# Kernel tuning notes

Hardware: AMD Instinct MI355X
Metric: run time of the kernel (lower is better)

The kernel has to match this reference:

```python
import jax, jax.numpy as jnp
import numpy as np

B, N, D, H = 1, 4096, 1024, 16
HD = D // H  # head_dim = 64


def setup_inputs() -> dict:
    key = jax.random.key(0)
    ks = jax.random.split(key, 5)
    s = 0.02
    return {
        "x": jax.random.normal(ks[0], (B, N, D), dtype=jnp.float32),
        "Wq": jax.random.normal(ks[1], (D, D), dtype=jnp.float32) * s,
        "Wk": jax.random.normal(ks[2], (D, D), dtype=jnp.float32) * s,
        "Wv": jax.random.normal(ks[3], (D, D), dtype=jnp.float32) * s,
        "Wo": jax.random.normal(ks[4], (D, D), dtype=jnp.float32) * s,
        "bo": jnp.zeros((D,), dtype=jnp.float32),
    }


def reference(x, Wq, Wk, Wv, Wo, bo):
    b, n, d = x.shape
    # QKV projections -> [b, h, n, hd]
    def proj(W):
        return jnp.einsum("bnd,de->bne", x, W).reshape(b, n, H, HD).transpose(0, 2, 1, 3)
    q, k, v = proj(Wq), proj(Wk), proj(Wv)
    # Scores [b, h, n, n] with causal mask (matches masked_fill with triu(diag=1))
    scores = jnp.einsum("bhqd,bhkd->bhqk", q, k)
    causal = jnp.tril(jnp.ones((n, n), dtype=bool))
    scores = jnp.where(causal, scores, -jnp.inf)
    attn = jax.nn.softmax(scores / jnp.sqrt(jnp.float32(HD)), axis=-1)
    # dropout p=0.0 -> identity
    ctx = jnp.einsum("bhqk,bhkd->bhqd", attn, v)
    ctx = ctx.transpose(0, 2, 1, 3).reshape(b, n, d)
    return jnp.einsum("bnd,de->bne", ctx, Wo) + bo
```

## Files before the change

kernel.cpp:

```cpp
#include <hip/hip_runtime.h>


#define N_TOK 4096
#define DMODEL 1024
#define NH 16
#define HDIM 64

typedef __bf16 bf16x8 __attribute__((ext_vector_type(8)));
typedef __bf16 bf16x2v __attribute__((ext_vector_type(2)));
typedef short short4v __attribute__((ext_vector_type(4)));
typedef unsigned int uint2v __attribute__((ext_vector_type(2)));
typedef float f32x4 __attribute__((ext_vector_type(4)));

__device__ __forceinline__ unsigned short f2bf(float f) {
  unsigned u = __builtin_bit_cast(unsigned, f);
  u += 0x7FFFu + ((u >> 16) & 1u);
  return (unsigned short)(u >> 16);
}

__device__ __forceinline__ float bf2f(unsigned short u) {
  unsigned x = (unsigned)u << 16;
  return __builtin_bit_cast(float, x);
}

__device__ __forceinline__ unsigned pack2bf(float f0, float f1) {
  unsigned a = __builtin_bit_cast(unsigned, f0);
  unsigned b = __builtin_bit_cast(unsigned, f1);
  a += 0x7FFFu + ((a >> 16) & 1u);
  b += 0x7FFFu + ((b >> 16) & 1u);
  return (a >> 16) | (b & 0xFFFF0000u);
}

__device__ __forceinline__ unsigned packpk(float f0, float f1) {
#if defined(__HIP_DEVICE_COMPILE__) && __has_builtin(__builtin_amdgcn_cvt_pk_bf16_f32)
  bf16x2v r = __builtin_amdgcn_cvt_pk_bf16_f32(f0, f1);
  return __builtin_bit_cast(unsigned, r);
#else
  return pack2bf(f0, f1);
#endif
}

__device__ __forceinline__ float fast_exp2(float x) {
#if defined(__HIP_DEVICE_COMPILE__)
#if __has_builtin(__builtin_amdgcn_exp2f)
  return __builtin_amdgcn_exp2f(x);
#else
  float r;
  asm("v_exp_f32 %0, %1" : "=v"(r) : "v"(x));
  return r;
#endif
#else
  return exp2f(x);
#endif
}

__device__ __forceinline__ f32x4 mfma16x16x16(short4v a, short4v b, f32x4 c) {
#if defined(__HIP_DEVICE_COMPILE__)
#if __has_builtin(__builtin_amdgcn_mfma_f32_16x16x16bf16_1k)
  return __builtin_amdgcn_mfma_f32_16x16x16bf16_1k(a, b, c, 0, 0, 0);
#else
  asm volatile("v_mfma_f32_16x16x16_bf16 %0, %1, %2, %0\n\ts_nop 7\n\ts_nop 1"
               : "+v"(c) : "v"(a), "v"(b));
  return c;
#endif
#else
  return c;
#endif
}

__device__ __forceinline__ void gll16(const unsigned short* g, unsigned short* l) {
#if defined(__HIP_DEVICE_COMPILE__)
  __builtin_amdgcn_global_load_lds((const __attribute__((address_space(1))) void*)g,
                                   (__attribute__((address_space(3))) void*)l, 16, 0, 0);
#endif
}

__global__ __launch_bounds__(256) void prep_kernel(
    const float* __restrict__ x, unsigned short* __restrict__ xb,
    const float* __restrict__ Wq, const float* __restrict__ Wk,
    const float* __restrict__ Wv, const float* __restrict__ Wo,
    unsigned short* __restrict__ Wqt, unsigned short* __restrict__ Wkt,
    unsigned short* __restrict__ Wvt, unsigned short* __restrict__ Wot) {
  const int bx = blockIdx.x;
  if (bx < 4096) {
    const int i = (bx * 256 + threadIdx.x) * 4;
    float4 v = *(const float4*)(x + i);
    ushort4 o;
    o.x = f2bf(v.x); o.y = f2bf(v.y); o.z = f2bf(v.z); o.w = f2bf(v.w);
    *(ushort4*)(xb + i) = o;
    return;
  }
  __shared__ float t[32][33];
  const int r = bx - 4096;
  const int z = r >> 10, rem = r & 1023;
  const int by = rem >> 5, bxx = rem & 31;
  const float* src;
  unsigned short* dst;
  switch (z) {
    case 0: src = Wq; dst = Wqt; break;
    case 1: src = Wk; dst = Wkt; break;
    case 2: src = Wv; dst = Wvt; break;
    default: src = Wo; dst = Wot; break;
  }
  const int tx = threadIdx.x & 31, ty = threadIdx.x >> 5;
  const int xx = bxx * 32 + tx;
  const int y0 = by * 32;
#pragma unroll
  for (int i = 0; i < 32; i += 8) t[ty + i][tx] = src[(y0 + ty + i) * DMODEL + xx];
  __syncthreads();
  const int ox = by * 32 + tx;
  const int oy0 = bxx * 32;
#pragma unroll
  for (int i = 0; i < 32; i += 8) dst[(oy0 + ty + i) * DMODEL + ox] = f2bf(t[tx][ty + i]);
}

__global__ __launch_bounds__(256) void gemm_qkv_kernel(
    const unsigned short* __restrict__ xb,
    const unsigned short* __restrict__ Wqt, const unsigned short* __restrict__ Wkt,
    const unsigned short* __restrict__ Wvt,
    unsigned short* __restrict__ Qg, unsigned short* __restrict__ Kg,
    unsigned short* __restrict__ Vtg) {
  __shared__ unsigned short As[128 * 32];
  __shared__ unsigned short Bs[128 * 32];
  __shared__ unsigned short Tt[64 * 132];
  const int z = blockIdx.z;
  const unsigned short* Bmat = (z == 0) ? Wqt : ((z == 1) ? Wkt : Wvt);
  const int tid = threadIdx.x, lane = tid & 63, wv = tid >> 6;
  const int quad = lane >> 4, l15 = lane & 15;
  const int wm = wv >> 1, wn = wv & 1;
  const int tm0 = blockIdx.y * 128, tn0 = blockIdx.x * 128;
  const int lrow = lane >> 2, lcol = (lane & 3) * 8;
  const f32x4 zero4 = {0.f, 0.f, 0.f, 0.f};
  f32x4 acc[4][4];
#pragma unroll
  for (int i = 0; i < 4; ++i)
#pragma unroll
    for (int j = 0; j < 4; ++j) acc[i][j] = zero4;

  for (int kb = 0; kb < DMODEL; kb += 32) {
#pragma unroll
    for (int r = 0; r < 2; ++r) {
      const int row0 = r * 64 + wv * 16;
      gll16(&xb[(tm0 + row0 + lrow) * DMODEL + kb + lcol], &As[row0 * 32]);
      gll16(&Bmat[(tn0 + row0 + lrow) * DMODEL + kb + lcol], &Bs[row0 * 32]);
    }
    __syncthreads();
    bf16x8 af[4], bfr[4];
#pragma unroll
    for (int i = 0; i < 4; ++i) {
      af[i]  = *(const bf16x8*)&As[(wm * 64 + i * 16 + l15) * 32 + quad * 8];
      bfr[i] = *(const bf16x8*)&Bs[(wn * 64 + i * 16 + l15) * 32 + quad * 8];
    }
#pragma unroll
    for (int mt = 0; mt < 4; ++mt)
#pragma unroll
      for (int nt = 0; nt < 4; ++nt)
        acc[mt][nt] = __builtin_amdgcn_mfma_f32_16x16x32_bf16(af[mt], bfr[nt], acc[mt][nt], 0, 0, 0);
    __syncthreads();
  }

  const float qs = 0.125f * 1.44269504088896f;
  if (z < 2) {
#pragma unroll
    for (int mt = 0; mt < 4; ++mt)
#pragma unroll
      for (int nt = 0; nt < 4; ++nt)
#pragma unroll
        for (int r = 0; r < 4; ++r) {
          const int row = tm0 + wm * 64 + mt * 16 + quad * 4 + r;
          const int col = tn0 + wn * 64 + nt * 16 + l15;
          const float v = acc[mt][nt][r];
          const int hh = col >> 6, hd = col & 63;
          if (z == 0) Qg[(hh * N_TOK + row) * HDIM + hd] = f2bf(v * qs);
          else        Kg[(hh * N_TOK + row) * HDIM + hd] = f2bf(v);
        }
  } else {
#pragma unroll 1
    for (int p = 0; p < 2; ++p) {
      if (wn == p) {
#pragma unroll
        for (int mt = 0; mt < 4; ++mt)
#pragma unroll
          for (int nt = 0; nt < 4; ++nt) {
            const int c = nt * 16 + l15;
#pragma unroll
            for (int r = 0; r < 4; ++r)
              Tt[c * 132 + wm * 64 + mt * 16 + quad * 4 + r] = f2bf(acc[mt][nt][r]);
          }
      }
      __syncthreads();
      const int c = tid >> 2, seg = tid & 3;
      const int hh = (tn0 + p * 64) >> 6;
      unsigned short* dst = Vtg + hh * (HDIM * N_TOK) + c * N_TOK + tm0 + seg * 32;
      const unsigned short* srcp = &Tt[c * 132 + seg * 32];
#pragma unroll
      for (int j = 0; j < 4; ++j)
        *(uint4*)(dst + j * 8) = *(const uint4*)(srcp + j * 8);
      __syncthreads();
    }
  }
}

#define TRW 68

__device__ static const unsigned char T_TAB[63] = {
    10, 11, 12, 13, 14, 15, 16, 17, 18, 19, 20, 21, 22, 23, 24, 25, 26, 27, 28, 29, 30,
    31, 21, 22, 23, 24, 25, 26, 27, 28, 29, 30, 31,
    9, 20, 31, 8, 19, 30, 7, 18, 29, 6, 17, 28, 5, 16, 27,
    4, 15, 26, 3, 14, 25, 2, 13, 24, 1, 12, 23, 0, 11, 22};
__device__ static const unsigned char G_TAB[63] = {
    0, 0, 0, 0, 0, 0, 0, 0, 0, 0, 0, 0, 0, 0, 0, 0, 0, 0, 0, 0, 0,
    0, 1, 1, 1, 1, 1, 1, 1, 1, 1, 1, 1,
    0, 1, 2, 0, 1, 2, 0, 1, 2, 0, 1, 2, 0, 1, 2,
    0, 1, 2, 0, 1, 2, 0, 1, 2, 0, 1, 2, 0, 1, 2};

__device__ __forceinline__ void stage_kv(
    const unsigned short* __restrict__ Kh, const unsigned short* __restrict__ Vh,
    int kv0, char* buf, int wv, int lane) {
  unsigned short* Ksb = (unsigned short*)buf;
  unsigned short* Vsb = (unsigned short*)(buf + 8192);
  const int r8 = lane >> 3, g = lane & 7;
  const int sw = ((g ^ r8) * 8);
  const int row = wv * 8;
  gll16(&Kh[(kv0 + row + r8) * HDIM + sw], &Ksb[row * 64]);
  gll16(&Vh[(row + r8) * N_TOK + kv0 + sw], &Vsb[row * 64]);
}

template <bool MASKED>
__device__ __forceinline__ void attn_step(
    int kvs, int qw, int quad, int l15,
    const unsigned short* __restrict__ Ks, const unsigned short* __restrict__ Vs,
    const bf16x8 (&qf)[2], f32x4 (&o)[4], float& l_) {
  const f32x4 zero4 = {0.f, 0.f, 0.f, 0.f};
  const int s = l15 & 7;
  const int g0 = (quad ^ s) * 8;
  f32x4 c[4];
#pragma unroll
  for (int mt = 0; mt < 4; ++mt) {
    const unsigned short* kp = &Ks[(mt * 16 + l15) * 64];
    const bf16x8 kf0 = *(const bf16x8*)(kp + g0);
    const bf16x8 kf1 = *(const bf16x8*)(kp + (g0 ^ 32));
    c[mt] = __builtin_amdgcn_mfma_f32_16x16x32_bf16(kf0, qf[0], zero4, 0, 0, 0);
    c[mt] = __builtin_amdgcn_mfma_f32_16x16x32_bf16(kf1, qf[1], c[mt], 0, 0, 0);
  }
  short4v pb[4];
  const int q = qw + l15;
  float ls = 0.f;
#pragma unroll
  for (int mt = 0; mt < 4; ++mt) {
    float p[4];
#pragma unroll
    for (int r = 0; r < 4; ++r) {
      float v = c[mt][r];
      if (MASKED) v = ((kvs + mt * 16 + quad * 4 + r) <= q) ? v : -3e38f;
      p[r] = fast_exp2(v);
    }
    ls += (p[0] + p[1]) + (p[2] + p[3]);
    uint2v w;
    w.x = packpk(p[0], p[1]);
    w.y = packpk(p[2], p[3]);
    pb[mt] = __builtin_bit_cast(short4v, w);
  }
  l_ += ls;
#pragma unroll
  for (int mt = 0; mt < 4; ++mt)
#pragma unroll
    for (int dt = 0; dt < 4; ++dt) {
      const int gv = (((2 * mt + (quad >> 1)) ^ s) * 8) + (quad & 1) * 4;
      const short4v vfx = *(const short4v*)&Vs[(dt * 16 + l15) * 64 + gv];
      o[dt] = mfma16x16x16(vfx, pb[mt], o[dt]);
    }
}

__global__ __launch_bounds__(512, 8) void attn_kernel(
    const unsigned short* __restrict__ Qg, const unsigned short* __restrict__ Kg,
    const unsigned short* __restrict__ Vtg, unsigned short* __restrict__ ctx,
    unsigned short* __restrict__ part_o, float* __restrict__ part_l) {
  __shared__ __align__(16) char smem[34816];
  const int tid = threadIdx.x, lane = tid & 63, wv = tid >> 6;
  const int quad = lane >> 4, l15 = lane & 15;

  const int u = blockIdx.x >> 4;
  const int h = blockIdx.x & 15;
  const int t = T_TAB[u], g = G_TAB[u];
  const int c0 = g * 11;
  const int cend = (c0 + 10 < t) ? (c0 + 10) : t;
  const int mlen = 2 * (cend - c0 + 1);
  const bool multi = (t >= 11);
  const int qb = t * 128, qw = qb + wv * 16;

  const unsigned short* Qh = Qg + h * N_TOK * HDIM;
  const unsigned short* Kh = Kg + h * N_TOK * HDIM;
  const unsigned short* Vh = Vtg + h * HDIM * N_TOK;

  bf16x8 qf[2];
#pragma unroll
  for (int hh = 0; hh < 2; ++hh)
    qf[hh] = *(const bf16x8*)&Qh[(qw + l15) * HDIM + hh * 32 + quad * 8];

  const f32x4 zero4 = {0.f, 0.f, 0.f, 0.f};
  f32x4 o[4];
#pragma unroll
  for (int dt = 0; dt < 4; ++dt) o[dt] = zero4;
  float l_ = 0.f;

  const int kvbase = c0 << 7;
  stage_kv(Kh, Vh, kvbase, smem, wv, lane);
  int cur = 0;
#pragma unroll 1
  for (int mc = 0; mc < mlen; ++mc) {
    const int kv0 = kvbase + mc * 64;
    __syncthreads();
    if (mc + 1 < mlen)
      stage_kv(Kh, Vh, kv0 + 64, smem + (cur ^ 1) * 16384, wv, lane);
    const unsigned short* Ksb = (const unsigned short*)(smem + cur * 16384);
    const unsigned short* Vsb = (const unsigned short*)(smem + cur * 16384 + 8192);
    if (kv0 <= qw + 15) {
      __builtin_amdgcn_s_setprio(1);
      if (kv0 + 63 <= qw)
        attn_step<false>(kv0, qw, quad, l15, Ksb, Vsb, qf, o, l_);
      else
        attn_step<true>(kv0, qw, quad, l15, Ksb, Vsb, qf, o, l_);
      __builtin_amdgcn_s_setprio(0);
    }
    cur ^= 1;
  }
  __syncthreads();

  float* Tr = (float*)(smem + wv * (16 * TRW * 4));
  const int tq = lane >> 2, seg = lane & 3;
  if (!multi) {
    float l = l_;
    l += __shfl_xor(l, 16, 64);
    l += __shfl_xor(l, 32, 64);
    const float inv = 1.0f / l;
#pragma unroll
    for (int dt = 0; dt < 4; ++dt) {
      f32x4 v = o[dt] * inv;
      *(f32x4*)&Tr[l15 * TRW + dt * 16 + quad * 4] = v;
    }
    unsigned short* dst = &ctx[(qb + wv * 16 + tq) * DMODEL + h * HDIM + seg * 16];
    const float* src = &Tr[tq * TRW + seg * 16];
#pragma unroll
    for (int j = 0; j < 2; ++j) {
      const float* s8 = src + j * 8;
      uint4 w;
      w.x = pack2bf(s8[0], s8[1]);
      w.y = pack2bf(s8[2], s8[3]);
      w.z = pack2bf(s8[4], s8[5]);
      w.w = pack2bf(s8[6], s8[7]);
      *(uint4*)(dst + j * 8) = w;
    }
  } else {
    const int slot = (h * 21 + (t - 11)) * 3 + g;
    float l = l_;
    l += __shfl_xor(l, 16, 64);
    l += __shfl_xor(l, 32, 64);
    if (quad == 0) part_l[slot * 128 + wv * 16 + l15] = l;
#pragma unroll
    for (int dt = 0; dt < 4; ++dt)
      *(f32x4*)&Tr[l15 * TRW + dt * 16 + quad * 4] = o[dt];
    unsigned short* dst = part_o + (size_t)slot * 8192 + (wv * 16 + tq) * 64 + seg * 16;
    const float* src = &Tr[tq * TRW + seg * 16];
#pragma unroll
    for (int j = 0; j < 2; ++j) {
      const float* s8 = src + j * 8;
      uint4 w;
      w.x = pack2bf(s8[0], s8[1]);
      w.y = pack2bf(s8[2], s8[3]);
      w.z = pack2bf(s8[4], s8[5]);
      w.w = pack2bf(s8[6], s8[7]);
      *(uint4*)(dst + j * 8) = w;
    }
  }
}

__global__ __launch_bounds__(256) void merge_kernel(
    const unsigned short* __restrict__ part_o, const float* __restrict__ part_l,
    unsigned short* __restrict__ ctx) {
  const int b = blockIdx.x;
  const int h = b / 21, tt = b % 21;
  const int t = tt + 11;
  const int ng = t / 11 + 1;
  const int tid = threadIdx.x;
  const int q = tid >> 1, half = tid & 1;
  const int s0 = (h * 21 + tt) * 3;
  float l = 0.f;
  for (int g = 0; g < ng; ++g) l += part_l[(s0 + g) * 128 + q];
  const float inv = 1.0f / l;
  unsigned short* dst = &ctx[(t * 128 + q) * DMODEL + h * HDIM + half * 32];
#pragma unroll
  for (int j = 0; j < 4; ++j) {
    float acc[8] = {0.f, 0.f, 0.f, 0.f, 0.f, 0.f, 0.f, 0.f};
    for (int g = 0; g < ng; ++g) {
      const uint4 w = *(const uint4*)(part_o + (size_t)(s0 + g) * 8192 + q * 64 + half * 32 + j * 8);
      const unsigned short* us = (const unsigned short*)&w;
#pragma unroll
      for (int e = 0; e < 8; ++e) acc[e] += bf2f(us[e]);
    }
    uint4 w;
    w.x = pack2bf(acc[0] * inv, acc[1] * inv);
    w.y = pack2bf(acc[2] * inv, acc[3] * inv);
    w.z = pack2bf(acc[4] * inv, acc[5] * inv);
    w.w = pack2bf(acc[6] * inv, acc[7] * inv);
    *(uint4*)(dst + j * 8) = w;
  }
}

__global__ __launch_bounds__(256) void gemm_out_kernel(
    const unsigned short* __restrict__ ctxb, const unsigned short* __restrict__ Wot,
    const float* __restrict__ bo, float* __restrict__ out) {
  __shared__ unsigned short As[128 * 32];
  __shared__ unsigned short Bs[128 * 32];
  const int tid = threadIdx.x, lane = tid & 63, wv = tid >> 6;
  const int quad = lane >> 4, l15 = lane & 15;
  const int wm = wv >> 1, wn = wv & 1;
  const int tm0 = blockIdx.y * 128, tn0 = blockIdx.x * 128;
  const int lrow = lane >> 2, lcol = (lane & 3) * 8;
  const f32x4 zero4 = {0.f, 0.f, 0.f, 0.f};
  f32x4 acc[4][4];
#pragma unroll
  for (int i = 0; i < 4; ++i)
#pragma unroll
    for (int j = 0; j < 4; ++j) acc[i][j] = zero4;

  for (int kb = 0; kb < DMODEL; kb += 32) {
#pragma unroll
    for (int r = 0; r < 2; ++r) {
      const int row0 = r * 64 + wv * 16;
      gll16(&ctxb[(tm0 + row0 + lrow) * DMODEL + kb + lcol], &As[row0 * 32]);
      gll16(&Wot[(tn0 + row0 + lrow) * DMODEL + kb + lcol], &Bs[row0 * 32]);
    }
    __syncthreads();
    bf16x8 af[4], bfr[4];
#pragma unroll
    for (int i = 0; i < 4; ++i) {
      af[i]  = *(const bf16x8*)&As[(wm * 64 + i * 16 + l15) * 32 + quad * 8];
      bfr[i] = *(const bf16x8*)&Bs[(wn * 64 + i * 16 + l15) * 32 + quad * 8];
    }
#pragma unroll
    for (int mt = 0; mt < 4; ++mt)
#pragma unroll
      for (int nt = 0; nt < 4; ++nt)
        acc[mt][nt] = __builtin_amdgcn_mfma_f32_16x16x32_bf16(af[mt], bfr[nt], acc[mt][nt], 0, 0, 0);
    __syncthreads();
  }
#pragma unroll
  for (int mt = 0; mt < 4; ++mt)
#pragma unroll
    for (int nt = 0; nt < 4; ++nt)
#pragma unroll
      for (int r = 0; r < 4; ++r) {
        const int row = tm0 + wm * 64 + mt * 16 + quad * 4 + r;
        const int col = tn0 + wn * 64 + nt * 16 + l15;
        out[row * DMODEL + col] = acc[mt][nt][r] + bo[col];
      }
}

extern "C" void kernel_launch(void* const* d_in, const int* in_sizes, int n_in,
                              void* d_out, int out_size, void* d_ws, size_t ws_size,
                              hipStream_t stream) {
  const float* x  = (const float*)d_in[0];
  const float* Wq = (const float*)d_in[1];
  const float* Wk = (const float*)d_in[2];
  const float* Wv = (const float*)d_in[3];
  const float* Wo = (const float*)d_in[4];
  const float* bo = (const float*)d_in[5];
  float* out = (float*)d_out;

  char* ws = (char*)d_ws;
  unsigned short* xb  = (unsigned short*)(ws);
  unsigned short* Wqt = (unsigned short*)(ws + 8388608);
  unsigned short* Wkt = (unsigned short*)(ws + 8388608 + 2097152);
  unsigned short* Wvt = (unsigned short*)(ws + 8388608 + 2 * 2097152);
  unsigned short* Wot = (unsigned short*)(ws + 8388608 + 3 * 2097152);
  unsigned short* Qg  = (unsigned short*)(ws + 16777216);
  unsigned short* Kg  = (unsigned short*)(ws + 25165824);
  unsigned short* Vtg = (unsigned short*)(ws + 33554432);
  unsigned short* ctx = xb;
  unsigned short* part_o = (unsigned short*)(ws + 41943040);
  float* part_l = (float*)(ws + 58458112);

  prep_kernel<<<8192, 256, 0, stream>>>(x, xb, Wq, Wk, Wv, Wo, Wqt, Wkt, Wvt, Wot);
  gemm_qkv_kernel<<<dim3(DMODEL / 128, N_TOK / 128, 3), 256, 0, stream>>>(xb, Wqt, Wkt, Wvt, Qg, Kg, Vtg);
  attn_kernel<<<1008, 512, 0, stream>>>(Qg, Kg, Vtg, ctx, part_o, part_l);
  merge_kernel<<<336, 256, 0, stream>>>(part_o, part_l, ctx);
  gemm_out_kernel<<<dim3(DMODEL / 128, N_TOK / 128), 256, 0, stream>>>(ctx, Wot, bo, out);
}
```

Before: 229.7 us.

## Rebalance split-KV attention into finer, evenly sized chunks of at most eight tiles

Causal attention work is now split so that each query tile t uses (t/8)+1 KV groups of near-equal size, instead of fixed 11-tile chunks. The scheduling tables are rebuilt for 80 work units per head and order the largest units first, raising the grid from 1008 to 1280 blocks. The goal is to shorten the longest-running block and reduce tail imbalance. In exchange, more partial outputs must be written and merged. Part of the partial buffer reuses the workspace of the already-consumed Wq/Wk/Wv transposes so the extra partials fit.

```diff
diff --git a/kernel.cpp b/kernel.cpp
--- a/kernel.cpp
+++ b/kernel.cpp
@@ -203,16 +203,37 @@
 
 #define TRW 68
 
-__device__ static const unsigned char T_TAB[63] = {
-    10, 11, 12, 13, 14, 15, 16, 17, 18, 19, 20, 21, 22, 23, 24, 25, 26, 27, 28, 29, 30,
-    31, 21, 22, 23, 24, 25, 26, 27, 28, 29, 30, 31,
-    9, 20, 31, 8, 19, 30, 7, 18, 29, 6, 17, 28, 5, 16, 27,
-    4, 15, 26, 3, 14, 25, 2, 13, 24, 1, 12, 23, 0, 11, 22};
-__device__ static const unsigned char G_TAB[63] = {
-    0, 0, 0, 0, 0, 0, 0, 0, 0, 0, 0, 0, 0, 0, 0, 0, 0, 0, 0, 0, 0,
-    0, 1, 1, 1, 1, 1, 1, 1, 1, 1, 1, 1,
-    0, 1, 2, 0, 1, 2, 0, 1, 2, 0, 1, 2, 0, 1, 2,
-    0, 1, 2, 0, 1, 2, 0, 1, 2, 0, 1, 2, 0, 1, 2};
+__device__ static const unsigned char T_TAB[80] = {
+    7, 14, 15, 15, 21, 22, 22, 23, 23, 23, 28, 29, 29, 30, 30, 30, 31, 31, 31, 31,
+    6, 12, 13, 13, 14, 18, 19, 19, 20, 20, 20, 21, 21, 22, 24, 25, 25, 26, 26, 26,
+    27, 27, 27, 27, 28, 28, 28, 29, 29, 30,
+    5, 10, 11, 11, 12, 16, 16, 17, 17, 17, 18, 18, 19, 24, 24, 24, 25, 25, 26,
+    4, 8, 9, 9, 10, 16,
+    3, 8,
+    2,
+    1,
+    0};
+__device__ static const unsigned char G_TAB[80] = {
+    0, 0, 0, 1, 0, 0, 1, 0, 1, 2, 0, 0, 1, 0, 1, 2, 0, 1, 2, 3,
+    0, 0, 0, 1, 1, 0, 0, 1, 0, 1, 2, 1, 2, 2, 0, 0, 1, 0, 1, 2,
+    0, 1, 2, 3, 1, 2, 3, 2, 3, 3,
+    0, 0, 0, 1, 1, 0, 1, 0, 1, 2, 1, 2, 2, 1, 2, 3, 2, 3, 3,
+    0, 0, 0, 1, 1, 2,
+    0, 1,
+    0,
+    0,
+    0};
+__device__ static const unsigned char PS_TAB[32] = {
+    0, 0, 0, 0, 0, 0, 0, 0,
+    0, 2, 4, 6, 8, 10, 12, 14,
+    16, 19, 22, 25, 28, 31, 34, 37,
+    40, 44, 48, 52, 56, 60, 64, 68};
+
+__device__ __forceinline__ unsigned short* part_slot_ptr(
+    unsigned short* poA, unsigned short* poB, int slot) {
+  return (slot < 384) ? poA + (size_t)slot * 8192
+                      : poB + (size_t)(slot - 384) * 8192;
+}
 
 __device__ __forceinline__ void stage_kv(
     const unsigned short* __restrict__ Kh, const unsigned short* __restrict__ Vh,
@@ -275,7 +296,8 @@
 __global__ __launch_bounds__(512, 8) void attn_kernel(
     const unsigned short* __restrict__ Qg, const unsigned short* __restrict__ Kg,
     const unsigned short* __restrict__ Vtg, unsigned short* __restrict__ ctx,
-    unsigned short* __restrict__ part_o, float* __restrict__ part_l) {
+    unsigned short* __restrict__ part_oA, unsigned short* __restrict__ part_oB,
+    float* __restrict__ part_l) {
   __shared__ __align__(16) char smem[34816];
   const int tid = threadIdx.x, lane = tid & 63, wv = tid >> 6;
   const int quad = lane >> 4, l15 = lane & 15;
@@ -283,10 +305,14 @@
   const int u = blockIdx.x >> 4;
   const int h = blockIdx.x & 15;
   const int t = T_TAB[u], g = G_TAB[u];
-  const int c0 = g * 11;
-  const int cend = (c0 + 10 < t) ? (c0 + 10) : t;
-  const int mlen = 2 * (cend - c0 + 1);
-  const bool multi = (t >= 11);
+  const int ng = (t >> 3) + 1;
+  const int tp1 = t + 1;
+  const int gbase = tp1 / ng;
+  const int grem = tp1 - gbase * ng;
+  const int s0 = g * gbase + (g < grem ? g : grem);
+  const int cnt = gbase + (g < grem ? 1 : 0);
+  const int mlen = 2 * cnt;
+  const bool multi = (t >= 8);
   const int qb = t * 128, qw = qb + wv * 16;
 
   const unsigned short* Qh = Qg + h * N_TOK * HDIM;
@@ -304,7 +330,7 @@
   for (int dt = 0; dt < 4; ++dt) o[dt] = zero4;
   float l_ = 0.f;
 
-  const int kvbase = c0 << 7;
+  const int kvbase = s0 << 7;
   stage_kv(Kh, Vh, kvbase, smem, wv, lane);
   int cur = 0;
 #pragma unroll 1
@@ -352,7 +378,7 @@
       *(uint4*)(dst + j * 8) = w;
     }
   } else {
-    const int slot = (h * 21 + (t - 11)) * 3 + g;
+    const int slot = h * 72 + PS_TAB[t] + g;
     float l = l_;
     l += __shfl_xor(l, 16, 64);
     l += __shfl_xor(l, 32, 64);
@@ -360,7 +386,8 @@
 #pragma unroll
     for (int dt = 0; dt < 4; ++dt)
       *(f32x4*)&Tr[l15 * TRW + dt * 16 + quad * 4] = o[dt];
-    unsigned short* dst = part_o + (size_t)slot * 8192 + (wv * 16 + tq) * 64 + seg * 16;
+    unsigned short* dst = part_slot_ptr(part_oA, part_oB, slot) +
+                          (wv * 16 + tq) * 64 + seg * 16;
     const float* src = &Tr[tq * TRW + seg * 16];
 #pragma unroll
     for (int j = 0; j < 2; ++j) {
@@ -376,24 +403,25 @@
 }
 
 __global__ __launch_bounds__(256) void merge_kernel(
-    const unsigned short* __restrict__ part_o, const float* __restrict__ part_l,
-    unsigned short* __restrict__ ctx) {
+    unsigned short* __restrict__ part_oA, unsigned short* __restrict__ part_oB,
+    const float* __restrict__ part_l, unsigned short* __restrict__ ctx) {
   const int b = blockIdx.x;
-  const int h = b / 21, tt = b % 21;
-  const int t = tt + 11;
-  const int ng = t / 11 + 1;
+  const int h = b / 24, tt = b - h * 24;
+  const int t = tt + 8;
+  const int ng = (t >> 3) + 1;
   const int tid = threadIdx.x;
   const int q = tid >> 1, half = tid & 1;
-  const int s0 = (h * 21 + tt) * 3;
+  const int slot0 = h * 72 + PS_TAB[t];
   float l = 0.f;
-  for (int g = 0; g < ng; ++g) l += part_l[(s0 + g) * 128 + q];
+  for (int g = 0; g < ng; ++g) l += part_l[(slot0 + g) * 128 + q];
   const float inv = 1.0f / l;
   unsigned short* dst = &ctx[(t * 128 + q) * DMODEL + h * HDIM + half * 32];
 #pragma unroll
   for (int j = 0; j < 4; ++j) {
     float acc[8] = {0.f, 0.f, 0.f, 0.f, 0.f, 0.f, 0.f, 0.f};
     for (int g = 0; g < ng; ++g) {
-      const uint4 w = *(const uint4*)(part_o + (size_t)(s0 + g) * 8192 + q * 64 + half * 32 + j * 8);
+      const unsigned short* po = part_slot_ptr(part_oA, part_oB, slot0 + g);
+      const uint4 w = *(const uint4*)(po + q * 64 + half * 32 + j * 8);
       const unsigned short* us = (const unsigned short*)&w;
 #pragma unroll
       for (int e = 0; e < 8; ++e) acc[e] += bf2f(us[e]);
@@ -478,12 +506,13 @@
   unsigned short* Kg  = (unsigned short*)(ws + 25165824);
   unsigned short* Vtg = (unsigned short*)(ws + 33554432);
   unsigned short* ctx = xb;
-  unsigned short* part_o = (unsigned short*)(ws + 41943040);
-  float* part_l = (float*)(ws + 58458112);
+  unsigned short* part_oA = (unsigned short*)(ws + 8388608);
+  unsigned short* part_oB = (unsigned short*)(ws + 41943040);
+  float* part_l = (float*)(ws + 54525952);
 
   prep_kernel<<<8192, 256, 0, stream>>>(x, xb, Wq, Wk, Wv, Wo, Wqt, Wkt, Wvt, Wot);
   gemm_qkv_kernel<<<dim3(DMODEL / 128, N_TOK / 128, 3), 256, 0, stream>>>(xb, Wqt, Wkt, Wvt, Qg, Kg, Vtg);
-  attn_kernel<<<1008, 512, 0, stream>>>(Qg, Kg, Vtg, ctx, part_o, part_l);
-  merge_kernel<<<336, 256, 0, stream>>>(part_o, part_l, ctx);
+  attn_kernel<<<1280, 512, 0, stream>>>(Qg, Kg, Vtg, ctx, part_oA, part_oB, part_l);
+  merge_kernel<<<384, 256, 0, stream>>>(part_oA, part_oB, part_l, ctx);
   gemm_out_kernel<<<dim3(DMODEL / 128, N_TOK / 128), 256, 0, stream>>>(ctx, Wot, bo, out);
 }
```

Result: no change. 233.0 us (+1.5%).
